# Performance work log

Measured on AMD Instinct MI355X. Metric: run time of the kernel, lower is better.

The kernel has to match this reference:

```python
import jax, jax.numpy as jnp
import numpy as np

B, S, D = 4, 2048, 1024
H = 4 * D          # expert hidden dim
E_SPEC = 4         # num specific experts
E_SHR = 2          # num shared experts
TOP_K = 2


def setup_inputs() -> dict:
    key = jax.random.key(0)
    ks = jax.random.split(key, 16)
    s = 0.02
    return {
        "x": jax.random.normal(ks[0], (B, S, D), jnp.float32),
        # specific experts (stacked over expert axis)
        "spec_w1": jax.random.normal(ks[1], (E_SPEC, D, H), jnp.float32) * s,
        "spec_b1": jnp.zeros((E_SPEC, H), jnp.float32),
        "spec_w2": jax.random.normal(ks[2], (E_SPEC, H, D), jnp.float32) * s,
        "spec_b2": jnp.zeros((E_SPEC, D), jnp.float32),
        "spec_rw": jax.random.normal(ks[3], (D, E_SPEC), jnp.float32) * s,
        "spec_rb": jnp.zeros((E_SPEC,), jnp.float32),
        # shared experts
        "shr_w1": jax.random.normal(ks[4], (E_SHR, D, H), jnp.float32) * s,
        "shr_b1": jnp.zeros((E_SHR, H), jnp.float32),
        "shr_w2": jax.random.normal(ks[5], (E_SHR, H, D), jnp.float32) * s,
        "shr_b2": jnp.zeros((E_SHR, D), jnp.float32),
        "shr_rw": jax.random.normal(ks[6], (D, E_SHR), jnp.float32) * s,
        "shr_rb": jnp.zeros((E_SHR,), jnp.float32),
    }


def _expert_mlp(xf, w1, b1, w2, b2):
    # xf: [T, D]; w1: [E, D, H]; w2: [E, H, D] -> [E, T, D]
    h = jax.nn.gelu(jnp.einsum("td,edh->eth", xf, w1) + b1[:, None, :],
                    approximate=False)
    return jnp.einsum("eth,ehd->etd", h, w2) + b2[:, None, :]


def reference(x, spec_w1, spec_b1, spec_w2, spec_b2, spec_rw, spec_rb,
              shr_w1, shr_b1, shr_w2, shr_b2, shr_rw, shr_rb):
    b, s, d = x.shape
    xf = x.reshape(-1, d)                      # [T, D]
    T = xf.shape[0]

    # --- specific (top-k) routing ---
    spec_probs = jax.nn.softmax(xf @ spec_rw + spec_rb, axis=-1)   # [T, E]
    topk_probs, topk_idx = jax.lax.top_k(spec_probs, TOP_K)        # [T, K]

    # aux load-balancing loss
    counts = jnp.zeros((E_SPEC,), jnp.float32).at[topk_idx.reshape(-1)].add(1.0)
    fraction = counts / (T * TOP_K)
    aux_loss = E_SPEC * jnp.sum(fraction * spec_probs.mean(axis=0))

    # gate[t, e] = sum_k topk_probs[t,k] * 1[topk_idx[t,k]==e]
    gate = jnp.sum(jax.nn.one_hot(topk_idx, E_SPEC, dtype=xf.dtype)
                   * topk_probs[..., None], axis=1)                # [T, E]

    spec_out_e = _expert_mlp(xf, spec_w1, spec_b1, spec_w2, spec_b2)  # [E, T, D]
    specific_out = jnp.einsum("te,etd->td", gate, spec_out_e)

    # --- shared (dense) experts ---
    shr_probs = jax.nn.softmax(xf @ shr_rw + shr_rb, axis=-1)      # [T, E_shr]
    shr_out_e = _expert_mlp(xf, shr_w1, shr_b1, shr_w2, shr_b2)    # [E_shr, T, D]
    shared_out = jnp.einsum("te,etd->td", shr_probs, shr_out_e)

    final = (specific_out + shared_out).reshape(b, s, d)
    return final, aux_loss
```

## Files before the change

kernel.cpp:

```cpp
#include <hip/hip_runtime.h>
#include <hip/hip_bf16.h>

#define T_TOK 8192
#define DDIM 1024
#define HDIM 4096

typedef __bf16 bf16;
typedef bf16 bf16x8 __attribute__((ext_vector_type(8)));
typedef float f32x4 __attribute__((ext_vector_type(4)));

#define ASM_VMCNT(n) asm volatile("s_waitcnt vmcnt(" #n ")" ::: "memory")
#define MFMA16(a, b, c) __builtin_amdgcn_mfma_f32_16x16x32_bf16((a), (b), (c), 0, 0, 0)

__device__ __forceinline__ void gl_lds16(const void* g, void* l) {
  __builtin_amdgcn_global_load_lds(
      (const __attribute__((address_space(1))) unsigned int*)g,
      (__attribute__((address_space(3))) unsigned int*)l, 16, 0, 0);
}

__device__ __forceinline__ float gelu_f(float v) {
  const float x = v * 0.7071067811865475f;
  const float ax = fabsf(x);
  const float t = 1.0f / fmaf(0.3275911f, ax, 1.0f);
  float p = fmaf(1.061405429f, t, -1.453152027f);
  p = fmaf(p, t, 1.421413741f);
  p = fmaf(p, t, -0.284496736f);
  p = fmaf(p, t, 0.254829592f);
  p = p * t;
  const float e = __expf(-ax * ax);
  const float er = fmaf(-p, e, 1.0f);
  const float erfx = (x >= 0.0f) ? er : -er;
  return 0.5f * v * (1.0f + erfx);
}

__global__ __launch_bounds__(256) void conv_router(
    const float* __restrict__ x, bf16* __restrict__ xb,
    const float* __restrict__ srw, const float* __restrict__ srb,
    const float* __restrict__ hrw, const float* __restrict__ hrb,
    float* __restrict__ gate, float4* __restrict__ probs4,
    int* __restrict__ top2) {
  const int lane = threadIdx.x & 63;
  const int w = threadIdx.x >> 6;
  const int t = blockIdx.x * 4 + w;

  const float* xr = x + (size_t)t * DDIM;
  bf16* xbr = xb + (size_t)t * DDIM;
  float p0 = 0, p1 = 0, p2 = 0, p3 = 0, p4 = 0, p5 = 0;
#pragma unroll
  for (int c = 0; c < 4; ++c) {
    const int d = c * 256 + lane * 4;
    const float4 xv = *(const float4*)(xr + d);
    bf16 ov[4] = {(bf16)xv.x, (bf16)xv.y, (bf16)xv.z, (bf16)xv.w};
    *(float2*)(xbr + d) = *(float2*)ov;
    const float xa[4] = {xv.x, xv.y, xv.z, xv.w};
#pragma unroll
    for (int j = 0; j < 4; ++j) {
      const float xd = xa[j];
      const float4 r4 = *(const float4*)(srw + (size_t)(d + j) * 4);
      p0 += xd * r4.x; p1 += xd * r4.y; p2 += xd * r4.z; p3 += xd * r4.w;
      const float2 r2 = *(const float2*)(hrw + (size_t)(d + j) * 2);
      p4 += xd * r2.x; p5 += xd * r2.y;
    }
  }
#pragma unroll
  for (int off = 32; off >= 1; off >>= 1) {
    p0 += __shfl_xor(p0, off);
    p1 += __shfl_xor(p1, off);
    p2 += __shfl_xor(p2, off);
    p3 += __shfl_xor(p3, off);
    p4 += __shfl_xor(p4, off);
    p5 += __shfl_xor(p5, off);
  }
  if (lane == 0) {
    const float l0 = p0 + srb[0], l1 = p1 + srb[1];
    const float l2 = p2 + srb[2], l3 = p3 + srb[3];
    const float m = fmaxf(fmaxf(l0, l1), fmaxf(l2, l3));
    const float e0 = expf(l0 - m), e1 = expf(l1 - m);
    const float e2 = expf(l2 - m), e3 = expf(l3 - m);
    const float s = e0 + e1 + e2 + e3;
    float pr[4] = {e0 / s, e1 / s, e2 / s, e3 / s};
    int i1 = 0; float v1 = pr[0];
#pragma unroll
    for (int e = 1; e < 4; ++e) if (pr[e] > v1) { v1 = pr[e]; i1 = e; }
    int i2 = -1; float v2 = -1.0f;
#pragma unroll
    for (int e = 0; e < 4; ++e)
      if (e != i1 && pr[e] > v2) { v2 = pr[e]; i2 = e; }
    float g[4] = {0, 0, 0, 0};
    g[i1] = v1; g[i2] = v2;
    float* gr = gate + (size_t)t * 8;
    gr[0] = g[0]; gr[1] = g[1]; gr[2] = g[2]; gr[3] = g[3];
    const float h0 = p4 + hrb[0], h1 = p5 + hrb[1];
    const float mh = fmaxf(h0, h1);
    const float q0 = expf(h0 - mh), q1 = expf(h1 - mh);
    const float qs = q0 + q1;
    gr[4] = q0 / qs; gr[5] = q1 / qs; gr[6] = 0; gr[7] = 0;
    probs4[t] = make_float4(pr[0], pr[1], pr[2], pr[3]);
    top2[t] = i1 | (i2 << 8);
  }
}

__global__ __launch_bounds__(256) void transpose_convert6(
    const float* __restrict__ spec_w, const float* __restrict__ shr_w,
    bf16* __restrict__ dst, int R, int C) {
  __shared__ float tile[32][33];
  const int z = blockIdx.z;
  const float* src = (z < 4) ? spec_w + (size_t)z * R * C
                             : shr_w + (size_t)(z - 4) * R * C;
  bf16* d = dst + (size_t)z * R * C;
  const int c0 = blockIdx.x * 32, r0 = blockIdx.y * 32;
  const int tx = threadIdx.x & 31, ty = threadIdx.x >> 5;
#pragma unroll
  for (int i = 0; i < 4; ++i)
    tile[ty + 8 * i][tx] = src[(size_t)(r0 + ty + 8 * i) * C + c0 + tx];
  __syncthreads();
#pragma unroll
  for (int i = 0; i < 4; ++i)
    d[(size_t)(c0 + ty + 8 * i) * R + r0 + tx] = (bf16)tile[tx][ty + 8 * i];
}

__global__ __launch_bounds__(1024) void scan_build(
    const int* __restrict__ top2, const float4* __restrict__ probs4,
    int* __restrict__ meta, int* __restrict__ lists,
    float* __restrict__ auxg) {
  __shared__ unsigned long long sc[1024];
  __shared__ float4 rp[512];
  const int tid = threadIdx.x;

  int ee[8];
  unsigned long long c = 0;
  float4 ps = make_float4(0.f, 0.f, 0.f, 0.f);
#pragma unroll
  for (int j = 0; j < 8; ++j) {
    const int t = tid * 8 + j;
    const int p = top2[t];
    ee[j] = p;
    const int a = p & 15, b = (p >> 8) & 15;
    c += (1ULL << (16 * a)) + (1ULL << (16 * b));
    const float4 pv = probs4[t];
    ps.x += pv.x; ps.y += pv.y; ps.z += pv.z; ps.w += pv.w;
  }
  sc[tid] = c;
  __syncthreads();
  for (int off = 1; off < 1024; off <<= 1) {
    const unsigned long long mine = sc[tid];
    const unsigned long long prev = (tid >= off) ? sc[tid - off] : 0ULL;
    __syncthreads();
    sc[tid] = mine + prev;
    __syncthreads();
  }
  const unsigned long long incl = sc[tid];
  const unsigned long long tot = sc[1023];
  const unsigned long long excl = incl - c;
  int q0 = (int)(excl & 0xffff), q1 = (int)((excl >> 16) & 0xffff);
  int q2 = (int)((excl >> 32) & 0xffff), q3 = (int)((excl >> 48) & 0xffff);
#pragma unroll
  for (int j = 0; j < 8; ++j) {
    const int t = tid * 8 + j;
    const int a = ee[j] & 15, b = (ee[j] >> 8) & 15;
    const int pa = (a == 0) ? q0 : (a == 1) ? q1 : (a == 2) ? q2 : q3;
    lists[a * 8192 + pa] = t;
    q0 += (a == 0); q1 += (a == 1); q2 += (a == 2); q3 += (a == 3);
    const int pb = (b == 0) ? q0 : (b == 1) ? q1 : (b == 2) ? q2 : q3;
    lists[b * 8192 + pb] = t;
    q0 += (b == 0); q1 += (b == 1); q2 += (b == 2); q3 += (b == 3);
  }
  if (tid == 1023) {
    const int c0 = (int)(tot & 0xffff), c1 = (int)((tot >> 16) & 0xffff);
    const int c2 = (int)((tot >> 32) & 0xffff), c3 = (int)((tot >> 48) & 0xffff);
    meta[24] = c0; meta[25] = c1; meta[26] = c2; meta[27] = c3;
    auxg[0] = (float)c0; auxg[1] = (float)c1;
    auxg[2] = (float)c2; auxg[3] = (float)c3;
    const int nb0 = (c0 + 255) >> 8, nb1 = (c1 + 255) >> 8;
    const int nb2 = (c2 + 255) >> 8, nb3 = (c3 + 255) >> 8;
    const int ch0 = (nb0 + 3) >> 2, ch1 = (nb1 + 3) >> 2;
    const int ch2 = (nb2 + 3) >> 2, ch3 = (nb3 + 3) >> 2;
    meta[0] = 0; meta[1] = 1024; meta[2] = 2048;
    meta[3] = 2048 + 128 * ch0;
    meta[4] = meta[3] + 128 * ch1;
    meta[5] = meta[4] + 128 * ch2;
    meta[6] = meta[5] + 128 * ch3;
    meta[8] = 0; meta[9] = 256; meta[10] = 512;
    meta[11] = 512 + 32 * ch0;
    meta[12] = meta[11] + 32 * ch1;
    meta[13] = meta[12] + 32 * ch2;
    meta[14] = meta[13] + 32 * ch3;
    meta[16] = 0; meta[17] = 8192; meta[18] = 16384;
    meta[19] = 16384 + nb0 * 256;
    meta[20] = meta[19] + nb1 * 256;
    meta[21] = meta[20] + nb2 * 256;
  }
  if (tid >= 512) rp[tid - 512] = ps;
  __syncthreads();
  if (tid < 512) {
    const float4 o = rp[tid];
    ps.x += o.x; ps.y += o.y; ps.z += o.z; ps.w += o.w;
  }
  for (int w = 256; w >= 1; w >>= 1) {
    __syncthreads();
    if (tid >= w && tid < 2 * w) rp[tid - w] = ps;
    __syncthreads();
    if (tid < w) {
      const float4 o = rp[tid];
      ps.x += o.x; ps.y += o.y; ps.z += o.z; ps.w += o.w;
    }
  }
  if (tid == 0) {
    auxg[4] = ps.x; auxg[5] = ps.y; auxg[6] = ps.z; auxg[7] = ps.w;
  }
}

__global__ void aux_finalize(const float* __restrict__ auxg,
                             float* __restrict__ outp) {
  float a = 0.0f;
#pragma unroll
  for (int e = 0; e < 4; ++e)
    a += (auxg[e] / (float)(T_TOK * 2)) * (auxg[4 + e] / (float)T_TOK);
  outp[0] = 4.0f * a;
}

__global__ __launch_bounds__(256, 2) void g1_batched(
    const bf16* __restrict__ A, const bf16* __restrict__ w1t,
    const float* __restrict__ spec_b1, const float* __restrict__ shr_b1,
    bf16* __restrict__ h_all, const int* __restrict__ meta,
    const int* __restrict__ lists, int s_only, int packed) {
  __shared__ __align__(1024) bf16 As[3 * 256 * 32];
  __shared__ __align__(1024) bf16 Bs[3 * 128 * 32];

  const int tid = threadIdx.x;
  const int lane = tid & 63, wid = tid >> 6;
  const int wm = wid >> 1, wn = wid & 1;
  const int lr = lane & 15, lg = lane >> 4;

  int s, local;
  if (s_only >= 0) {
    s = s_only; local = blockIdx.x;
  } else {
    const int b = blockIdx.x;
    if (b >= meta[6]) return;
    s = 0;
#pragma unroll
    for (int i = 1; i < 6; ++i) s += (b >= meta[i]);
    local = b - meta[s];
  }

  int bm, bn, nbm = 32;
  if (s < 2) {
    if (local >= 1024) return;
    const int xcd = local & 7, idx = local >> 3;
    bm = (xcd >> 1) * 8 + idx / 16;
    bn = (xcd & 1) * 16 + idx % 16;
  } else {
    nbm = (meta[24 + s - 2] + 255) >> 8;
    const int CHm = (nbm + 3) >> 2;
    if (local >= 8 * CHm * 16) return;
    const int xc = local & 7, idx = local >> 3;
    bm = (xc >> 1) * CHm + idx / 16;
    bn = (xc & 1) * 16 + idx % 16;
    if (bm >= nbm) return;
  }
  const int hb = packed ? meta[16 + s] : 0;
  const bf16* B = w1t + (size_t)(s < 2 ? 4 + s : s - 2) * DDIM * HDIM;
  const float* bias = (s < 2) ? shr_b1 + (size_t)s * HDIM
                              : spec_b1 + (size_t)(s - 2) * HDIM;
  const int K = DDIM, N = HDIM;

  const int rl = tid >> 2;
  const int c = ((tid & 3) * 16) ^ (((rl >> 1) & 3) << 4);
  int ar0 = bm * 256 + rl, ar1 = ar0 + 64, ar2 = ar0 + 128, ar3 = ar0 + 192;
  if (s >= 2) {
    const int* lp = lists + (s - 2) * 8192;
    int t;
    t = lp[ar0]; ar0 = t < 0 ? 0 : t;
    t = lp[ar1]; ar1 = t < 0 ? 0 : t;
    t = lp[ar2]; ar2 = t < 0 ? 0 : t;
    t = lp[ar3]; ar3 = t < 0 ? 0 : t;
  }
  const bf16* sA0 = A + (size_t)ar0 * K + (c >> 1);
  const bf16* sA1 = A + (size_t)ar1 * K + (c >> 1);
  const bf16* sA2 = A + (size_t)ar2 * K + (c >> 1);
  const bf16* sA3 = A + (size_t)ar3 * K + (c >> 1);
  const bf16* sB0 = B + (size_t)(bn * 128 + rl) * K + (c >> 1);
  const bf16* sB1 = B + (size_t)(bn * 128 + 64 + rl) * K + (c >> 1);

  char* const dA = (char*)As + wid * 1024;
  char* const dB = (char*)Bs + wid * 1024;

  const int rkey = ((lr >> 1) & 3) << 4;
  const char* Ard = (const char*)As + (wm * 128 + lr) * 64 + ((lg * 16) ^ rkey);
  const char* Brd = (const char*)Bs + (wn * 64 + lr) * 64 + ((lg * 16) ^ rkey);

  f32x4 acc[8][4] = {};
  const int NT = K >> 5;

#define GW_STAGE(KO, SLOT)                         \
  gl_lds16(sA0 + (KO), dA + (SLOT)*16384);         \
  gl_lds16(sA1 + (KO), dA + (SLOT)*16384 + 4096);  \
  gl_lds16(sA2 + (KO), dA + (SLOT)*16384 + 8192);  \
  gl_lds16(sA3 + (KO), dA + (SLOT)*16384 + 12288); \
  gl_lds16(sB0 + (KO), dB + (SLOT)*8192);          \
  gl_lds16(sB1 + (KO), dB + (SLOT)*8192 + 4096);
  GW_STAGE(0, 0)
  GW_STAGE(32, 1)
  GW_STAGE(64, 2)
  ASM_VMCNT(12);
  __builtin_amdgcn_s_barrier();

#define GW_ITER(KT, SLOT)                                                  \
  {                                                                        \
    bf16x8 af[8], bfr[4];                                                  \
    _Pragma("unroll") for (int mf = 0; mf < 8; ++mf)                       \
        af[mf] = *(const bf16x8*)(Ard + (SLOT)*16384 + mf * 1024);         \
    _Pragma("unroll") for (int nf = 0; nf < 4; ++nf)                       \
        bfr[nf] = *(const bf16x8*)(Brd + (SLOT)*8192 + nf * 1024);         \
    asm volatile("s_waitcnt lgkmcnt(0)" ::: "memory");                     \
    __builtin_amdgcn_s_setprio(1);                                         \
    _Pragma("unroll") for (int mf = 0; mf < 8; ++mf)                       \
        _Pragma("unroll") for (int nf = 0; nf < 4; ++nf)                   \
            acc[mf][nf] = MFMA16(af[mf], bfr[nf], acc[mf][nf]);            \
    __builtin_amdgcn_s_setprio(0);                                         \
    __builtin_amdgcn_s_barrier();                                          \
    if ((KT) + 3 < NT) {                                                   \
      const int ko_ = ((KT) + 3) << 5;                                     \
      GW_STAGE(ko_, SLOT)                                                  \
      ASM_VMCNT(12);                                                       \
    } else if ((KT) + 2 < NT) {                                            \
      ASM_VMCNT(6);                                                        \
    } else if ((KT) + 1 < NT) {                                            \
      ASM_VMCNT(0);                                                        \
    }                                                                      \
    __builtin_amdgcn_s_barrier();                                          \
  }

  for (int kt0 = 0; kt0 < NT; kt0 += 3) {
    GW_ITER(kt0, 0)
    if (kt0 + 1 < NT) GW_ITER(kt0 + 1, 1)
    if (kt0 + 2 < NT) GW_ITER(kt0 + 2, 2)
  }

  const int colb = bn * 128 + wn * 64;
  const int rowb = hb + bm * 256 + wm * 128 + lg * 4;
  float bv[4];
#pragma unroll
  for (int nf = 0; nf < 4; ++nf) bv[nf] = bias[colb + nf * 16 + lr];
#pragma unroll
  for (int mf = 0; mf < 8; ++mf)
#pragma unroll
    for (int nf = 0; nf < 4; ++nf) {
      const int col = colb + nf * 16 + lr;
#pragma unroll
      for (int r = 0; r < 4; ++r) {
        const int row = rowb + mf * 16 + r;
        h_all[(size_t)row * N + col] = (bf16)gelu_f(acc[mf][nf][r] + bv[nf]);
      }
    }
}

__global__ __launch_bounds__(512, 2) void g2_batched(
    const bf16* __restrict__ h_all, const bf16* __restrict__ w2t,
    const float* __restrict__ spec_b2, const float* __restrict__ shr_b2,
    float* __restrict__ out, const float* __restrict__ gate,
    const int* __restrict__ meta, const int* __restrict__ lists,
    int s_only, int packed) {
  __shared__ __align__(1024) bf16 Alds[2 * 256 * 64];
  __shared__ __align__(1024) bf16 Blds[2 * 128 * 64];

  const int tid = threadIdx.x;
  const int lane = tid & 63, wid = tid >> 6;
  const int wm = wid >> 2, wn = wid & 3;
  const int lr = lane & 15, lg = lane >> 4;

  int s, local;
  if (s_only >= 0) {
    s = s_only; local = blockIdx.x;
  } else {
    const int b = blockIdx.x;
    if (b >= meta[14]) return;
    s = 0;
#pragma unroll
    for (int i = 9; i < 14; ++i) s += (b >= meta[i]);
    local = b - meta[8 + s];
  }

  int bm, bn, nbm = 32;
  if (s < 2) {
    if (local >= 256) return;
    const int xcd = local & 7, idx = local >> 3;
    bm = (xcd >> 1) * 8 + idx / 4;
    bn = (xcd & 1) * 4 + idx % 4;
  } else {
    nbm = (meta[24 + s - 2] + 255) >> 8;
    const int CHm = (nbm + 3) >> 2;
    if (local >= 8 * CHm * 4) return;
    const int xc = local & 7, idx = local >> 3;
    bm = (xc >> 1) * CHm + idx / 4;
    bn = (xc & 1) * 4 + idx % 4;
    if (bm >= nbm) return;
  }
  const int hb = packed ? meta[16 + s] : 0;
  const bf16* B = w2t + (size_t)(s < 2 ? 4 + s : s - 2) * DDIM * HDIM;
  const float* bias = (s < 2) ? shr_b2 + (size_t)s * DDIM
                              : spec_b2 + (size_t)(s - 2) * DDIM;
  const int gidx = (s < 2) ? 4 + s : s - 2;
  const int K = HDIM, N = DDIM;
  const int NT = K >> 6;

  const int L = tid * 16;
  const int rl = L >> 7;
  const int colb = (L & 127) ^ ((rl & 7) << 4);

  const int ar0 = hb + bm * 256 + rl;
  const bf16* sAc0 = h_all + (size_t)ar0 * K + (colb >> 1);
  const bf16* sAc1 = h_all + (size_t)(ar0 + 64) * K + (colb >> 1);
  const bf16* sAc2 = h_all + (size_t)(ar0 + 128) * K + (colb >> 1);
  const bf16* sAc3 = h_all + (size_t)(ar0 + 192) * K + (colb >> 1);
  const bf16* sB = B + (size_t)(bn * 128 + rl) * K + (colb >> 1);

  char* const ldsA = (char*)Alds;
  char* const ldsB = (char*)Blds;
  const int wb = wid * 1024;
  char* const stA[2] = {ldsA + wb, ldsA + 32768 + wb};
  char* const stB[2] = {ldsB + wb, ldsB + 16384 + wb};

  const int ax0 = (lg * 16) ^ ((lr & 7) << 4);
  const int ax1 = ax0 ^ 64;
  const int aro = (wm * 128 + lr) * 128;
  const int bro = (wn * 32 + lr) * 128;
  const char* const Ak0[2] = {ldsA + aro + ax0, ldsA + 32768 + aro + ax0};
  const char* const Ak1[2] = {ldsA + aro + ax1, ldsA + 32768 + aro + ax1};
  const char* const Bk0[2] = {ldsB + bro + ax0, ldsB + 16384 + bro + ax0};
  const char* const Bk1[2] = {ldsB + bro + ax1, ldsB + 16384 + bro + ax1};

  f32x4 acc[8][2] = {};

  gl_lds16(sAc0, stA[0]);
  gl_lds16(sAc1, stA[0] + 8192);
  gl_lds16(sAc2, stA[0] + 16384);
  gl_lds16(sAc3, stA[0] + 24576);
  gl_lds16(sB, stB[0]);
  gl_lds16(sB + (size_t)64 * K, stB[0] + 8192);
  gl_lds16(sB + 64, stB[1]);
  gl_lds16(sB + (size_t)64 * K + 64, stB[1] + 8192);
  gl_lds16(sAc0 + 64, stA[1]);
  gl_lds16(sAc1 + 64, stA[1] + 8192);
  ASM_VMCNT(4);
  __builtin_amdgcn_s_barrier();

  for (int kt0 = 0; kt0 < NT; kt0 += 2) {
#pragma unroll
    for (int par = 0; par < 2; ++par) {
      const int kt = kt0 + par;
      const int cur = par, oth = par ^ 1;
      const bool st1 = (kt + 1) < NT, st2 = (kt + 2) < NT;
      const size_t ko1 = (size_t)(kt + 1) << 6, ko2 = (size_t)(kt + 2) << 6;
      const char* Ac0 = Ak0[cur]; const char* Ac1 = Ak1[cur];
      const char* Bc0 = Bk0[cur]; const char* Bc1 = Bk1[cur];

      bf16x8 af[4][2], bfr[2][2];

#pragma unroll
      for (int mf = 0; mf < 4; ++mf) {
        af[mf][0] = *(const bf16x8*)(Ac0 + mf * 2048);
        af[mf][1] = *(const bf16x8*)(Ac1 + mf * 2048);
      }
      bfr[0][0] = *(const bf16x8*)(Bc0);
      bfr[0][1] = *(const bf16x8*)(Bc1);
      if (st1) {
        gl_lds16(sAc2 + ko1, stA[oth] + 16384);
        gl_lds16(sAc3 + ko1, stA[oth] + 24576);
      }
      __builtin_amdgcn_s_barrier();
      asm volatile("s_waitcnt lgkmcnt(0)" ::: "memory");
      __builtin_amdgcn_sched_barrier(0);
      __builtin_amdgcn_s_setprio(1);
#pragma unroll
      for (int mf = 0; mf < 4; ++mf) {
        acc[mf][0] = MFMA16(af[mf][0], bfr[0][0], acc[mf][0]);
        acc[mf][0] = MFMA16(af[mf][1], bfr[0][1], acc[mf][0]);
      }
      __builtin_amdgcn_s_setprio(0);
      __builtin_amdgcn_s_barrier();

      bfr[1][0] = *(const bf16x8*)(Bc0 + 2048);
      bfr[1][1] = *(const bf16x8*)(Bc1 + 2048);
      __builtin_amdgcn_s_barrier();
      asm volatile("s_waitcnt lgkmcnt(0)" ::: "memory");
      __builtin_amdgcn_sched_barrier(0);
      __builtin_amdgcn_s_setprio(1);
#pragma unroll
      for (int mf = 0; mf < 4; ++mf) {
        acc[mf][1] = MFMA16(af[mf][0], bfr[1][0], acc[mf][1]);
        acc[mf][1] = MFMA16(af[mf][1], bfr[1][1], acc[mf][1]);
      }
      __builtin_amdgcn_s_setprio(0);
      __builtin_amdgcn_s_barrier();

#pragma unroll
      for (int mf = 0; mf < 4; ++mf) {
        af[mf][0] = *(const bf16x8*)(Ac0 + 8192 + mf * 2048);
        af[mf][1] = *(const bf16x8*)(Ac1 + 8192 + mf * 2048);
      }
      if (st2) {
        gl_lds16(sB + ko2, stB[cur]);
        gl_lds16(sB + (size_t)64 * K + ko2, stB[cur] + 8192);
      }
      __builtin_amdgcn_s_barrier();
      asm volatile("s_waitcnt lgkmcnt(0)" ::: "memory");
      __builtin_amdgcn_sched_barrier(0);
      __builtin_amdgcn_s_setprio(1);
#pragma unroll
      for (int mf = 0; mf < 4; ++mf) {
        acc[4 + mf][0] = MFMA16(af[mf][0], bfr[0][0], acc[4 + mf][0]);
        acc[4 + mf][0] = MFMA16(af[mf][1], bfr[0][1], acc[4 + mf][0]);
      }
      __builtin_amdgcn_s_setprio(0);
      __builtin_amdgcn_s_barrier();

      if (st2) {
        gl_lds16(sAc0 + ko2, stA[cur]);
        gl_lds16(sAc1 + ko2, stA[cur] + 8192);
      }
      __builtin_amdgcn_s_setprio(1);
#pragma unroll
      for (int mf = 0; mf < 4; ++mf) {
        acc[4 + mf][1] = MFMA16(af[mf][0], bfr[1][0], acc[4 + mf][1]);
        acc[4 + mf][1] = MFMA16(af[mf][1], bfr[1][1], acc[4 + mf][1]);
      }
      __builtin_amdgcn_s_setprio(0);
      if (st2) {
        ASM_VMCNT(4);
        __builtin_amdgcn_s_barrier();
      } else if (st1) {
        ASM_VMCNT(0);
        __builtin_amdgcn_s_barrier();
      }
    }
  }

  const int colb2 = bn * 128 + wn * 32;
  const int rowb = bm * 256 + wm * 128 + lg * 4;
  float bv[2];
#pragma unroll
  for (int nf = 0; nf < 2; ++nf) bv[nf] = bias[colb2 + nf * 16 + lr];
#pragma unroll
  for (int mf = 0; mf < 8; ++mf) {
    int tok[4]; float gv[4];
#pragma unroll
    for (int r = 0; r < 4; ++r) {
      const int lrow = rowb + mf * 16 + r;
      tok[r] = (s < 2) ? lrow : lists[(s - 2) * 8192 + lrow];
      gv[r] = tok[r] >= 0 ? gate[(size_t)tok[r] * 8 + gidx] : 0.0f;
    }
#pragma unroll
    for (int nf = 0; nf < 2; ++nf) {
      const int col = colb2 + nf * 16 + lr;
#pragma unroll
      for (int r = 0; r < 4; ++r) {
        if (tok[r] >= 0) {
          const float v = acc[mf][nf][r] + bv[nf];
          atomicAdd(&out[(size_t)tok[r] * N + col], gv[r] * v);
        }
      }
    }
  }
}

extern "C" void kernel_launch(void* const* d_in, const int* in_sizes, int n_in,
                              void* d_out, int out_size, void* d_ws,
                              size_t ws_size, hipStream_t stream) {
  const float* x = (const float*)d_in[0];
  const float* spec_w1 = (const float*)d_in[1];
  const float* spec_b1 = (const float*)d_in[2];
  const float* spec_w2 = (const float*)d_in[3];
  const float* spec_b2 = (const float*)d_in[4];
  const float* spec_rw = (const float*)d_in[5];
  const float* spec_rb = (const float*)d_in[6];
  const float* shr_w1 = (const float*)d_in[7];
  const float* shr_b1 = (const float*)d_in[8];
  const float* shr_w2 = (const float*)d_in[9];
  const float* shr_b2 = (const float*)d_in[10];
  const float* shr_rw = (const float*)d_in[11];
  const float* shr_rb = (const float*)d_in[12];
  float* out = (float*)d_out;

  char* ws = (char*)d_ws;
  const size_t OFF_W1 = 16777216;
  const size_t OFF_W2 = OFF_W1 + 50331648;
  const size_t OFF_GATE = OFF_W2 + 50331648;
  const size_t OFF_AUX = OFF_GATE + 262144;
  const size_t OFF_META = OFF_AUX + 256;
  const size_t OFF_LIST = OFF_META + 256;
  const size_t OFF_T2 = OFF_LIST + 131072;
  const size_t OFF_P4 = OFF_T2 + 32768;
  const size_t OFF_H = OFF_P4 + 131072 + 1024;
  bf16* xb = (bf16*)ws;
  bf16* w1t = (bf16*)(ws + OFF_W1);
  bf16* w2t = (bf16*)(ws + OFF_W2);
  float* gate = (float*)(ws + OFF_GATE);
  float* auxg = (float*)(ws + OFF_AUX);
  int* meta = (int*)(ws + OFF_META);
  int* lists = (int*)(ws + OFF_LIST);
  int* top2 = (int*)(ws + OFF_T2);
  float4* probs4 = (float4*)(ws + OFF_P4);
  bf16* h_all = (bf16*)(ws + OFF_H);

  const size_t H_GRAND = (size_t)34048 * HDIM * 2;
  const bool grand = ws_size >= OFF_H + H_GRAND;

  hipMemsetAsync(out, 0, (size_t)T_TOK * DDIM * 4, stream);
  hipMemsetAsync(lists, 0xFF, 4 * 8192 * 4, stream);

  conv_router<<<T_TOK / 4, 256, 0, stream>>>(x, xb, spec_rw, spec_rb, shr_rw,
                                             shr_rb, gate, probs4, top2);
  scan_build<<<1, 1024, 0, stream>>>(top2, probs4, meta, lists, auxg);

  transpose_convert6<<<dim3(HDIM / 32, DDIM / 32, 6), 256, 0, stream>>>(
      spec_w1, shr_w1, w1t, DDIM, HDIM);
  transpose_convert6<<<dim3(DDIM / 32, HDIM / 32, 6), 256, 0, stream>>>(
      spec_w2, shr_w2, w2t, HDIM, DDIM);

  if (grand) {
    g1_batched<<<5120, 256, 0, stream>>>(xb, w1t, spec_b1, shr_b1, h_all,
                                         meta, lists, -1, 1);
    g2_batched<<<1280, 512, 0, stream>>>(h_all, w2t, spec_b2, shr_b2, out,
                                         gate, meta, lists, -1, 1);
  } else {
    for (int s = 0; s < 6; ++s) {
      g1_batched<<<1024, 256, 0, stream>>>(xb, w1t, spec_b1, shr_b1, h_all,
                                           meta, lists, s, 0);
      g2_batched<<<256, 512, 0, stream>>>(h_all, w2t, spec_b2, shr_b2, out,
                                          gate, meta, lists, s, 0);
    }
  }
  aux_finalize<<<1, 1, 0, stream>>>(auxg, out + (size_t)T_TOK * DDIM);
}
```

Baseline: 1.105 ms.

## Replace atomic scatter with ordered per-expert accumulation and fuse shared-expert GEMMs

The single batched up/down-projection launches are split into templated kernels. The two shared experts run as one wide first GEMM (N=8192), and their second GEMMs write the output directly: the first overwrites, the second accumulates. The four specific experts' second GEMMs then run as separate launches that add into the output with plain read-modify-write, so the output memset and all atomicAdds go away. In exchange, the per-expert down-projection launches are serialized and each may be small (about 128 blocks), which risks leaving CUs idle and adding launch gaps.

```diff
diff --git a/kernel.cpp b/kernel.cpp
--- a/kernel.cpp
+++ b/kernel.cpp
@@ -175,20 +175,15 @@
     const int nb2 = (c2 + 255) >> 8, nb3 = (c3 + 255) >> 8;
     const int ch0 = (nb0 + 3) >> 2, ch1 = (nb1 + 3) >> 2;
     const int ch2 = (nb2 + 3) >> 2, ch3 = (nb3 + 3) >> 2;
-    meta[0] = 0; meta[1] = 1024; meta[2] = 2048;
-    meta[3] = 2048 + 128 * ch0;
-    meta[4] = meta[3] + 128 * ch1;
-    meta[5] = meta[4] + 128 * ch2;
-    meta[6] = meta[5] + 128 * ch3;
-    meta[8] = 0; meta[9] = 256; meta[10] = 512;
-    meta[11] = 512 + 32 * ch0;
-    meta[12] = meta[11] + 32 * ch1;
-    meta[13] = meta[12] + 32 * ch2;
-    meta[14] = meta[13] + 32 * ch3;
-    meta[16] = 0; meta[17] = 8192; meta[18] = 16384;
-    meta[19] = 16384 + nb0 * 256;
-    meta[20] = meta[19] + nb1 * 256;
-    meta[21] = meta[20] + nb2 * 256;
+    meta[28] = 0;
+    meta[29] = 128 * ch0;
+    meta[30] = meta[29] + 128 * ch1;
+    meta[31] = meta[30] + 128 * ch2;
+    meta[32] = meta[31] + 128 * ch3;
+    meta[34] = 0;
+    meta[35] = nb0 * 256;
+    meta[36] = meta[35] + nb1 * 256;
+    meta[37] = meta[36] + nb2 * 256;
   }
   if (tid >= 512) rp[tid - 512] = ps;
   __syncthreads();
@@ -219,11 +214,12 @@
   outp[0] = 4.0f * a;
 }
 
-__global__ __launch_bounds__(256, 2) void g1_batched(
-    const bf16* __restrict__ A, const bf16* __restrict__ w1t,
-    const float* __restrict__ spec_b1, const float* __restrict__ shr_b1,
-    bf16* __restrict__ h_all, const int* __restrict__ meta,
-    const int* __restrict__ lists, int s_only, int packed) {
+template <int KIND>
+__global__ __launch_bounds__(256, 2) void g1k(
+    const bf16* __restrict__ A, const bf16* __restrict__ B,
+    const float* __restrict__ bias, bf16* __restrict__ h_all, int N,
+    int NCN, int CH_M, int CH_N, const int* __restrict__ meta,
+    const int* __restrict__ lists, int e) {
   __shared__ __align__(1024) bf16 As[3 * 256 * 32];
   __shared__ __align__(1024) bf16 Bs[3 * 128 * 32];
 
@@ -232,44 +228,44 @@
   const int wm = wid >> 1, wn = wid & 1;
   const int lr = lane & 15, lg = lane >> 4;
 
-  int s, local;
-  if (s_only >= 0) {
-    s = s_only; local = blockIdx.x;
-  } else {
+  int bm, bn, hb = 0, s = e;
+  const bf16* Bp = B;
+  const float* biasp = bias;
+  if constexpr (KIND == 0) {
+    const int xcd = blockIdx.x & 7, idx = blockIdx.x >> 3;
+    bm = (xcd / NCN) * CH_M + idx / CH_N;
+    bn = (xcd % NCN) * CH_N + idx % CH_N;
+  } else if constexpr (KIND == 1) {
     const int b = blockIdx.x;
-    if (b >= meta[6]) return;
-    s = 0;
-#pragma unroll
-    for (int i = 1; i < 6; ++i) s += (b >= meta[i]);
-    local = b - meta[s];
-  }
-
-  int bm, bn, nbm = 32;
-  if (s < 2) {
-    if (local >= 1024) return;
-    const int xcd = local & 7, idx = local >> 3;
-    bm = (xcd >> 1) * 8 + idx / 16;
-    bn = (xcd & 1) * 16 + idx % 16;
-  } else {
-    nbm = (meta[24 + s - 2] + 255) >> 8;
+    if (b >= meta[32]) return;
+    s = (b >= meta[29]) + (b >= meta[30]) + (b >= meta[31]);
+    const int local = b - meta[28 + s];
+    const int nbm = (meta[24 + s] + 255) >> 8;
     const int CHm = (nbm + 3) >> 2;
     if (local >= 8 * CHm * 16) return;
     const int xc = local & 7, idx = local >> 3;
     bm = (xc >> 1) * CHm + idx / 16;
     bn = (xc & 1) * 16 + idx % 16;
     if (bm >= nbm) return;
-  }
-  const int hb = packed ? meta[16 + s] : 0;
-  const bf16* B = w1t + (size_t)(s < 2 ? 4 + s : s - 2) * DDIM * HDIM;
-  const float* bias = (s < 2) ? shr_b1 + (size_t)s * HDIM
-                              : spec_b1 + (size_t)(s - 2) * HDIM;
-  const int K = DDIM, N = HDIM;
+    hb = meta[34 + s];
+    Bp = B + (size_t)s * DDIM * HDIM;
+    biasp = bias + (size_t)s * HDIM;
+  } else {
+    const int nbm = (meta[24 + e] + 255) >> 8;
+    const int CHm = (nbm + 3) >> 2;
+    if (blockIdx.x >= 8 * CHm * 16) return;
+    const int xc = blockIdx.x & 7, idx = blockIdx.x >> 3;
+    bm = (xc >> 1) * CHm + idx / 16;
+    bn = (xc & 1) * 16 + idx % 16;
+    if (bm >= nbm) return;
+  }
+  const int K = DDIM;
 
   const int rl = tid >> 2;
   const int c = ((tid & 3) * 16) ^ (((rl >> 1) & 3) << 4);
   int ar0 = bm * 256 + rl, ar1 = ar0 + 64, ar2 = ar0 + 128, ar3 = ar0 + 192;
-  if (s >= 2) {
-    const int* lp = lists + (s - 2) * 8192;
+  if constexpr (KIND != 0) {
+    const int* lp = lists + s * 8192;
     int t;
     t = lp[ar0]; ar0 = t < 0 ? 0 : t;
     t = lp[ar1]; ar1 = t < 0 ? 0 : t;
@@ -280,8 +276,8 @@
   const bf16* sA1 = A + (size_t)ar1 * K + (c >> 1);
   const bf16* sA2 = A + (size_t)ar2 * K + (c >> 1);
   const bf16* sA3 = A + (size_t)ar3 * K + (c >> 1);
-  const bf16* sB0 = B + (size_t)(bn * 128 + rl) * K + (c >> 1);
-  const bf16* sB1 = B + (size_t)(bn * 128 + 64 + rl) * K + (c >> 1);
+  const bf16* sB0 = Bp + (size_t)(bn * 128 + rl) * K + (c >> 1);
+  const bf16* sB1 = Bp + (size_t)(bn * 128 + 64 + rl) * K + (c >> 1);
 
   char* const dA = (char*)As + wid * 1024;
   char* const dB = (char*)Bs + wid * 1024;
@@ -342,7 +338,7 @@
   const int rowb = hb + bm * 256 + wm * 128 + lg * 4;
   float bv[4];
 #pragma unroll
-  for (int nf = 0; nf < 4; ++nf) bv[nf] = bias[colb + nf * 16 + lr];
+  for (int nf = 0; nf < 4; ++nf) bv[nf] = biasp[colb + nf * 16 + lr];
 #pragma unroll
   for (int mf = 0; mf < 8; ++mf)
 #pragma unroll
@@ -356,12 +352,12 @@
     }
 }
 
-__global__ __launch_bounds__(512, 2) void g2_batched(
-    const bf16* __restrict__ h_all, const bf16* __restrict__ w2t,
-    const float* __restrict__ spec_b2, const float* __restrict__ shr_b2,
-    float* __restrict__ out, const float* __restrict__ gate,
-    const int* __restrict__ meta, const int* __restrict__ lists,
-    int s_only, int packed) {
+template <int EMODE>
+__global__ __launch_bounds__(512, 2) void g2k(
+    const bf16* __restrict__ A, int lda, const bf16* __restrict__ B,
+    const float* __restrict__ bias, float* __restrict__ out,
+    const float* __restrict__ gate, int gidx, const int* __restrict__ meta,
+    const int* __restrict__ lists, int e, int packed) {
   __shared__ __align__(1024) bf16 Alds[2 * 256 * 64];
   __shared__ __align__(1024) bf16 Blds[2 * 128 * 64];
 
@@ -370,38 +366,21 @@
   const int wm = wid >> 2, wn = wid & 3;
   const int lr = lane & 15, lg = lane >> 4;
 
-  int s, local;
-  if (s_only >= 0) {
-    s = s_only; local = blockIdx.x;
-  } else {
-    const int b = blockIdx.x;
-    if (b >= meta[14]) return;
-    s = 0;
-#pragma unroll
-    for (int i = 9; i < 14; ++i) s += (b >= meta[i]);
-    local = b - meta[8 + s];
-  }
-
-  int bm, bn, nbm = 32;
-  if (s < 2) {
-    if (local >= 256) return;
-    const int xcd = local & 7, idx = local >> 3;
-    bm = (xcd >> 1) * 8 + idx / 4;
-    bn = (xcd & 1) * 4 + idx % 4;
-  } else {
-    nbm = (meta[24 + s - 2] + 255) >> 8;
+  int bm, bn, hb = 0;
+  if constexpr (EMODE == 3) {
+    const int nbm = (meta[24 + e] + 255) >> 8;
     const int CHm = (nbm + 3) >> 2;
-    if (local >= 8 * CHm * 4) return;
-    const int xc = local & 7, idx = local >> 3;
+    if (blockIdx.x >= 8 * CHm * 4) return;
+    const int xc = blockIdx.x & 7, idx = blockIdx.x >> 3;
     bm = (xc >> 1) * CHm + idx / 4;
     bn = (xc & 1) * 4 + idx % 4;
     if (bm >= nbm) return;
-  }
-  const int hb = packed ? meta[16 + s] : 0;
-  const bf16* B = w2t + (size_t)(s < 2 ? 4 + s : s - 2) * DDIM * HDIM;
-  const float* bias = (s < 2) ? shr_b2 + (size_t)s * DDIM
-                              : spec_b2 + (size_t)(s - 2) * DDIM;
-  const int gidx = (s < 2) ? 4 + s : s - 2;
+    hb = packed ? meta[34 + e] : 0;
+  } else {
+    const int xcd = blockIdx.x & 7, idx = blockIdx.x >> 3;
+    bm = (xcd >> 1) * 8 + idx / 4;
+    bn = (xcd & 1) * 4 + idx % 4;
+  }
   const int K = HDIM, N = DDIM;
   const int NT = K >> 6;
 
@@ -410,10 +389,10 @@
   const int colb = (L & 127) ^ ((rl & 7) << 4);
 
   const int ar0 = hb + bm * 256 + rl;
-  const bf16* sAc0 = h_all + (size_t)ar0 * K + (colb >> 1);
-  const bf16* sAc1 = h_all + (size_t)(ar0 + 64) * K + (colb >> 1);
-  const bf16* sAc2 = h_all + (size_t)(ar0 + 128) * K + (colb >> 1);
-  const bf16* sAc3 = h_all + (size_t)(ar0 + 192) * K + (colb >> 1);
+  const bf16* sAc0 = A + (size_t)ar0 * lda + (colb >> 1);
+  const bf16* sAc1 = A + (size_t)(ar0 + 64) * lda + (colb >> 1);
+  const bf16* sAc2 = A + (size_t)(ar0 + 128) * lda + (colb >> 1);
+  const bf16* sAc3 = A + (size_t)(ar0 + 192) * lda + (colb >> 1);
   const bf16* sB = B + (size_t)(bn * 128 + rl) * K + (colb >> 1);
 
   char* const ldsA = (char*)Alds;
@@ -544,21 +523,41 @@
   for (int nf = 0; nf < 2; ++nf) bv[nf] = bias[colb2 + nf * 16 + lr];
 #pragma unroll
   for (int mf = 0; mf < 8; ++mf) {
-    int tok[4]; float gv[4];
-#pragma unroll
-    for (int r = 0; r < 4; ++r) {
-      const int lrow = rowb + mf * 16 + r;
-      tok[r] = (s < 2) ? lrow : lists[(s - 2) * 8192 + lrow];
-      gv[r] = tok[r] >= 0 ? gate[(size_t)tok[r] * 8 + gidx] : 0.0f;
-    }
-#pragma unroll
-    for (int nf = 0; nf < 2; ++nf) {
-      const int col = colb2 + nf * 16 + lr;
+    if constexpr (EMODE != 3) {
+      float gv[4];
+#pragma unroll
+      for (int r = 0; r < 4; ++r)
+        gv[r] = gate[(size_t)(rowb + mf * 16 + r) * 8 + gidx];
+#pragma unroll
+      for (int nf = 0; nf < 2; ++nf) {
+        const int col = colb2 + nf * 16 + lr;
+#pragma unroll
+        for (int r = 0; r < 4; ++r) {
+          const float v = acc[mf][nf][r] + bv[nf];
+          const size_t oi = (size_t)(rowb + mf * 16 + r) * N + col;
+          if constexpr (EMODE == 1)
+            out[oi] += gv[r] * v;
+          else
+            out[oi] = gv[r] * v;
+        }
+      }
+    } else {
+      const int* lp = lists + e * 8192;
+      int tok[4]; float gv[4];
 #pragma unroll
       for (int r = 0; r < 4; ++r) {
-        if (tok[r] >= 0) {
-          const float v = acc[mf][nf][r] + bv[nf];
-          atomicAdd(&out[(size_t)tok[r] * N + col], gv[r] * v);
+        tok[r] = lp[rowb + mf * 16 + r];
+        gv[r] = tok[r] >= 0 ? gate[(size_t)tok[r] * 8 + gidx] : 0.0f;
+      }
+#pragma unroll
+      for (int nf = 0; nf < 2; ++nf) {
+        const int col = colb2 + nf * 16 + lr;
+#pragma unroll
+        for (int r = 0; r < 4; ++r) {
+          if (tok[r] >= 0) {
+            const float v = acc[mf][nf][r] + bv[nf];
+            out[(size_t)tok[r] * N + col] += gv[r] * v;
+          }
         }
       }
     }
@@ -584,6 +583,7 @@
   float* out = (float*)d_out;
 
   char* ws = (char*)d_ws;
+  const size_t DH = (size_t)DDIM * HDIM;
   const size_t OFF_W1 = 16777216;
   const size_t OFF_W2 = OFF_W1 + 50331648;
   const size_t OFF_GATE = OFF_W2 + 50331648;
@@ -602,12 +602,10 @@
   int* lists = (int*)(ws + OFF_LIST);
   int* top2 = (int*)(ws + OFF_T2);
   float4* probs4 = (float4*)(ws + OFF_P4);
-  bf16* h_all = (bf16*)(ws + OFF_H);
-
-  const size_t H_GRAND = (size_t)34048 * HDIM * 2;
-  const bool grand = ws_size >= OFF_H + H_GRAND;
-
-  hipMemsetAsync(out, 0, (size_t)T_TOK * DDIM * 4, stream);
+  bf16* h = (bf16*)(ws + OFF_H);
+
+  const bool rich = ws_size >= OFF_H + (size_t)17408 * HDIM * 2;
+
   hipMemsetAsync(lists, 0xFF, 4 * 8192 * 4, stream);
 
   conv_router<<<T_TOK / 4, 256, 0, stream>>>(x, xb, spec_rw, spec_rb, shr_rw,
@@ -619,18 +617,41 @@
   transpose_convert6<<<dim3(DDIM / 32, HDIM / 32, 6), 256, 0, stream>>>(
       spec_w2, shr_w2, w2t, HDIM, DDIM);
 
-  if (grand) {
-    g1_batched<<<5120, 256, 0, stream>>>(xb, w1t, spec_b1, shr_b1, h_all,
-                                         meta, lists, -1, 1);
-    g2_batched<<<1280, 512, 0, stream>>>(h_all, w2t, spec_b2, shr_b2, out,
-                                         gate, meta, lists, -1, 1);
+  if (rich) {
+    g1k<0><<<2048, 256, 0, stream>>>(xb, w1t + 4 * DH, shr_b1, h, 8192,
+                                     4, 16, 16, meta, lists, 0);
+    g2k<0><<<256, 512, 0, stream>>>(h, 8192, w2t + 4 * DH, shr_b2, out,
+                                    gate, 4, meta, lists, 0, 0);
+    g2k<1><<<256, 512, 0, stream>>>(h + 4096, 8192, w2t + 5 * DH,
+                                    shr_b2 + 1024, out, gate, 5, meta,
+                                    lists, 0, 0);
+    g1k<1><<<4096, 256, 0, stream>>>(xb, w1t, spec_b1, h, 4096,
+                                     2, 8, 16, meta, lists, 0);
+    for (int e = 0; e < 4; ++e)
+      g2k<3><<<256, 512, 0, stream>>>(h, 4096, w2t + (size_t)e * DH,
+                                      spec_b2 + (size_t)e * DDIM, out, gate,
+                                      e, meta, lists, e, 1);
   } else {
-    for (int s = 0; s < 6; ++s) {
-      g1_batched<<<1024, 256, 0, stream>>>(xb, w1t, spec_b1, shr_b1, h_all,
-                                           meta, lists, s, 0);
-      g2_batched<<<256, 512, 0, stream>>>(h_all, w2t, spec_b2, shr_b2, out,
-                                          gate, meta, lists, s, 0);
+    for (int es = 0; es < 2; ++es) {
+      g1k<0><<<1024, 256, 0, stream>>>(xb, w1t + (4 + es) * DH,
+                                       shr_b1 + (size_t)es * HDIM, h, 4096,
+                                       2, 8, 16, meta, lists, 0);
+      if (es == 0)
+        g2k<0><<<256, 512, 0, stream>>>(h, 4096, w2t + 4 * DH, shr_b2, out,
+                                        gate, 4, meta, lists, 0, 0);
+      else
+        g2k<1><<<256, 512, 0, stream>>>(h, 4096, w2t + 5 * DH,
+                                        shr_b2 + 1024, out, gate, 5, meta,
+                                        lists, 0, 0);
     }
+    for (int e = 0; e < 4; ++e) {
+      g1k<2><<<1024, 256, 0, stream>>>(xb, w1t + (size_t)e * DH,
+                                       spec_b1 + (size_t)e * HDIM, h, 4096,
+                                       2, 8, 16, meta, lists, e);
+      g2k<3><<<256, 512, 0, stream>>>(h, 4096, w2t + (size_t)e * DH,
+                                      spec_b2 + (size_t)e * DDIM, out, gate,
+                                      e, meta, lists, e, 0);
+    }
   }
   aux_finalize<<<1, 1, 0, stream>>>(auxg, out + (size_t)T_TOK * DDIM);
 }
```

After: 1.019 ms. 1.08x faster.
